# Optimization experiments

Measured on AMD Instinct MI355X. Metric: run time of the kernel, lower is better.

The kernel has to match this reference:

```python
import jax, jax.numpy as jnp
import numpy as np

NEG_INF = -1e9


def setup_inputs() -> dict:
    key = jax.random.key(0)
    ks = jax.random.split(key, 8)
    B, S, D = 8, 2048, 1024
    scale = 1.0 / np.sqrt(D)
    src = jax.random.normal(ks[0], (B, S, D), dtype=jnp.float32)
    pad_len = jax.random.randint(ks[1], (B,), 0, S // 10)
    pos = jnp.arange(S)[None, :]
    src_padding_mask = jnp.where(pos >= (S - pad_len)[:, None], NEG_INF, 0.0).astype(jnp.float32)[:, :, None]
    # causal (subsequent) additive mask [S,S]
    src_subsq_mask = jnp.where(jnp.triu(jnp.ones((S, S), dtype=bool), k=1), NEG_INF, 0.0).astype(jnp.float32)
    Wk = jax.random.normal(ks[2], (D, D), dtype=jnp.float32) * scale
    Wv = jax.random.normal(ks[3], (D, D), dtype=jnp.float32) * scale
    Wq = jax.random.normal(ks[4], (D, D), dtype=jnp.float32) * scale
    bk = jnp.zeros((D,), dtype=jnp.float32)
    bv = jnp.zeros((D,), dtype=jnp.float32)
    bq = jnp.zeros((D,), dtype=jnp.float32)
    return {"src": src, "src_padding_mask": src_padding_mask, "src_subsq_mask": src_subsq_mask,
            "Wk": Wk, "bk": bk, "Wv": Wv, "bv": bv, "Wq": Wq, "bq": bq}


def reference(src, src_padding_mask, src_subsq_mask, Wk, bk, Wv, bv, Wq, bq):
    d_model = src.shape[-1]
    # torch nn.Linear: x @ W.T + b
    keys = jnp.einsum('bsd,ed->bse', src, Wk) + bk
    values = jnp.einsum('bsd,ed->bse', src, Wv) + bv
    queries = jnp.einsum('bsd,ed->bse', src, Wq) + bq
    sqrt_d = jnp.asarray(d_model, src.dtype) ** 0.5
    att = jnp.einsum('bqd,bkd->bqk', queries, keys) / sqrt_d   # [B,S,S]
    att = att + jnp.swapaxes(src_padding_mask, 1, 2)           # [B,1,S] broadcast
    att = att + src_subsq_mask[None, :, :]                      # [1,S,S] broadcast
    att_softmax = jax.nn.softmax(att, axis=2)
    att_out = jnp.einsum('bqk,bkd->bqd', att_softmax, values)
    return att_out
```

## Files before the change

### kernel.cpp

```cpp
#include <hip/hip_runtime.h>
#include <cstdint>
#include <cstddef>

#define BATCH 8
#define SEQ   2048
#define DM    1024

typedef _Float16 half8 __attribute__((ext_vector_type(8)));
typedef _Float16 half4v __attribute__((ext_vector_type(4)));
typedef float floatx4 __attribute__((ext_vector_type(4)));
typedef float float4v __attribute__((ext_vector_type(4)));

#define GLOBAL_AS __attribute__((address_space(1)))
#define LDS_AS    __attribute__((address_space(3)))

__device__ __forceinline__ void gl_lds16(const _Float16* g, _Float16* l) {
    __builtin_amdgcn_global_load_lds((const GLOBAL_AS void*)g, (LDS_AS void*)l, 16, 0, 0);
}

__device__ __forceinline__ void stage128(const _Float16* __restrict__ g, int ld, int k0,
                                         _Float16* l, int wave, int lane) {
    const int rw = wave * 8 + (lane >> 3);
    const int sl = lane & 7;
    #pragma unroll
    for (int i = 0; i < 2; i++) {
        const int r = i * 64 + rw;
        gl_lds16(g + (size_t)r * ld + k0 + ((sl ^ (r & 7)) << 3),
                 l + ((i * 64 + wave * 8) << 6));
    }
}

#define LDA4(BUF, HALFOFF)                                                    \
    _Pragma("unroll")                                                         \
    for (int i = 0; i < 4; i++) {                                             \
        a[i][0] = *(const half8*)&SA[BUF][aoff + (HALFOFF) + i * 1024 + sl0]; \
        a[i][1] = *(const half8*)&SA[BUF][aoff + (HALFOFF) + i * 1024 + sl1]; \
    }
#define LDB2(DST, BUF, HALFOFF)                                               \
    _Pragma("unroll")                                                         \
    for (int j = 0; j < 2; j++) {                                             \
        DST[j][0] = *(const half8*)&SB[BUF][boff + (HALFOFF) + j * 4096 + sl0]; \
        DST[j][1] = *(const half8*)&SB[BUF][boff + (HALFOFF) + j * 4096 + sl1]; \
    }

#define PH_MFMA(IOFF, JOFF, BREG)                                             \
    __builtin_amdgcn_s_barrier();                                             \
    asm volatile("s_waitcnt lgkmcnt(0)" ::: "memory");                        \
    __builtin_amdgcn_s_setprio(1);                                            \
    _Pragma("unroll")                                                         \
    for (int i = 0; i < 4; i++) {                                             \
        _Pragma("unroll")                                                     \
        for (int j = 0; j < 2; j++) {                                         \
            acc[(IOFF) + i][(JOFF) + j] = __builtin_amdgcn_mfma_f32_16x16x32_f16( \
                a[i][0], BREG[j][0], acc[(IOFF) + i][(JOFF) + j], 0, 0, 0);   \
            acc[(IOFF) + i][(JOFF) + j] = __builtin_amdgcn_mfma_f32_16x16x32_f16( \
                a[i][1], BREG[j][1], acc[(IOFF) + i][(JOFF) + j], 0, 0, 0);   \
        }                                                                     \
    }                                                                         \
    __builtin_amdgcn_s_setprio(0);

__device__ __forceinline__ void gemm256_8ph(
    const _Float16* __restrict__ A, const _Float16* __restrict__ B,
    int lda, int ldb, int nkt,
    _Float16 (&SA)[2][16384], _Float16 (&SB)[2][16384],
    floatx4 (&acc)[8][4])
{
    const int t = threadIdx.x;
    const int wave = t >> 6, lane = t & 63;
    const int l15 = lane & 15, kq = lane >> 4;
    const int wm = wave >> 2, wn = wave & 3;

    const int aoff = (wm * 64 + l15) << 6;
    const int boff = (wn * 16 + l15) << 6;
    const int sl0 = ((kq ^ (l15 & 7)) << 3);
    const int sl1 = (((4 + kq) ^ (l15 & 7)) << 3);

    const _Float16* A128 = A + (size_t)128 * lda;
    const _Float16* B128 = B + (size_t)128 * ldb;

    stage128(A,    lda, 0,  &SA[0][0],    wave, lane);
    stage128(B,    ldb, 0,  &SB[0][0],    wave, lane);
    stage128(A128, lda, 0,  &SA[0][8192], wave, lane);
    stage128(B128, ldb, 0,  &SB[0][8192], wave, lane);
    stage128(A,    lda, 64, &SA[1][0],    wave, lane);
    stage128(B,    ldb, 64, &SB[1][0],    wave, lane);
    asm volatile("s_waitcnt vmcnt(4)" ::: "memory");
    __builtin_amdgcn_s_barrier();
    __builtin_amdgcn_sched_barrier(0);

    half8 a[4][2], b0[2][2], b1[2][2];

    for (int kt = 0; kt < nkt; kt += 2) {
        const bool more = (kt + 2) < nkt;
        const int kA = (kt + 1) * 64, kB = (kt + 2) * 64, kC = (kt + 3) * 64;

        LDA4(0, 0); LDB2(b0, 0, 0);
        stage128(A128, lda, kA, &SA[1][8192], wave, lane);
        PH_MFMA(0, 0, b0);
        __builtin_amdgcn_s_barrier();

        LDB2(b1, 0, 8192);
        stage128(B128, ldb, kA, &SB[1][8192], wave, lane);
        PH_MFMA(0, 2, b1);
        __builtin_amdgcn_s_barrier();

        LDA4(0, 8192);
        if (more) stage128(A, lda, kB, &SA[0][0], wave, lane);
        PH_MFMA(4, 0, b0);
        __builtin_amdgcn_s_barrier();

        if (more) stage128(B, ldb, kB, &SB[0][0], wave, lane);
        PH_MFMA(4, 2, b1);
        if (more) { asm volatile("s_waitcnt vmcnt(4)" ::: "memory"); }
        else      { asm volatile("s_waitcnt vmcnt(0)" ::: "memory"); }
        __builtin_amdgcn_s_barrier();
        __builtin_amdgcn_sched_barrier(0);

        LDA4(1, 0); LDB2(b0, 1, 0);
        if (more) stage128(A128, lda, kB, &SA[0][8192], wave, lane);
        PH_MFMA(0, 0, b0);
        __builtin_amdgcn_s_barrier();

        LDB2(b1, 1, 8192);
        if (more) stage128(B128, ldb, kB, &SB[0][8192], wave, lane);
        PH_MFMA(0, 2, b1);
        __builtin_amdgcn_s_barrier();

        LDA4(1, 8192);
        if (more) stage128(A, lda, kC, &SA[1][0], wave, lane);
        PH_MFMA(4, 0, b0);
        __builtin_amdgcn_s_barrier();

        if (more) stage128(B, ldb, kC, &SB[1][0], wave, lane);
        PH_MFMA(4, 2, b1);
        if (more) { asm volatile("s_waitcnt vmcnt(4)" ::: "memory"); }
        __builtin_amdgcn_s_barrier();
        __builtin_amdgcn_sched_barrier(0);
    }
}

__global__ __launch_bounds__(256) void convert_inputs(
    const float* __restrict__ src,
    const float* __restrict__ Wk, const float* __restrict__ Wv, const float* __restrict__ Wq,
    _Float16* __restrict__ Xh, _Float16* __restrict__ Wh)
{
    const int gid = blockIdx.x * 256 + threadIdx.x;
    const int gs  = gridDim.x * 256;
    const int nX4 = BATCH * SEQ * DM / 4;
    const int nW4 = DM * DM / 4;
    const float4v* s4  = (const float4v*)src;
    const float4v* wk4 = (const float4v*)Wk;
    const float4v* wv4 = (const float4v*)Wv;
    const float4v* wq4 = (const float4v*)Wq;
    half4v* x4 = (half4v*)Xh;
    half4v* w4 = (half4v*)Wh;
    for (int i = gid; i < nX4; i += gs) {
        float4v v = s4[i];
        half4v h;
        #pragma unroll
        for (int e = 0; e < 4; e++) h[e] = (_Float16)v[e];
        x4[i] = h;
    }
    for (int i = gid; i < nW4; i += gs) {
        float4v a = wk4[i], b = wv4[i], c = wq4[i];
        half4v ha, hb, hc;
        #pragma unroll
        for (int e = 0; e < 4; e++) { ha[e] = (_Float16)a[e]; hb[e] = (_Float16)b[e]; hc[e] = (_Float16)c[e]; }
        w4[i]           = ha;
        w4[nW4 + i]     = hb;
        w4[2 * nW4 + i] = hc;
    }
}

__global__ __launch_bounds__(512, 2) void qkv_gemm(
    const _Float16* __restrict__ Xh, const _Float16* __restrict__ Wh,
    const float* __restrict__ bk, const float* __restrict__ bv, const float* __restrict__ bq,
    _Float16* __restrict__ Kh, _Float16* __restrict__ Vt, _Float16* __restrict__ Qh)
{
    __shared__ __align__(16) _Float16 SA[2][16384];
    __shared__ __align__(16) _Float16 SB[2][16384];
    const int L = blockIdx.x;
    const int lid = (L & 7) * 96 + (L >> 3);
    const int z = lid >> 8;
    const int r = lid & 255;
    int by, bx;
    const _Float16 *A, *B;
    if (z == 1) {
        by = r & 3; bx = r >> 2;
        A = Wh + (size_t)DM * DM + (size_t)by * 256 * DM;
        B = Xh + (size_t)bx * 256 * DM;
    } else {
        by = r >> 2; bx = r & 3;
        A = Xh + (size_t)by * 256 * DM;
        B = Wh + (z ? (size_t)2 * DM * DM : (size_t)0) + (size_t)bx * 256 * DM;
    }
    floatx4 acc[8][4] = {};
    gemm256_8ph(A, B, DM, DM, 16, SA, SB, acc);

    const int t = threadIdx.x, wave = t >> 6, lane = t & 63;
    const int l15 = lane & 15, kq = lane >> 4;
    const int wm = wave >> 2, wn = wave & 3;
    if (z == 1) {
        #pragma unroll
        for (int i = 0; i < 8; i++)
            #pragma unroll
            for (int j = 0; j < 4; j++)
                #pragma unroll
                for (int rr = 0; rr < 4; rr++) {
                    const int d  = by * 256 + wm * 64 + (i & 3) * 16 + (i >> 2) * 128 + kq * 4 + rr;
                    const int sg = bx * 256 + wn * 16 + j * 64 + l15;
                    const int b = sg >> 11, s = sg & (SEQ - 1);
                    Vt[((size_t)b * DM + d) * SEQ + s] = (_Float16)(acc[i][j][rr] + bv[d]);
                }
    } else {
        const float* bias = z ? bq : bk;
        _Float16* outp    = z ? Qh : Kh;
        #pragma unroll
        for (int i = 0; i < 8; i++)
            #pragma unroll
            for (int j = 0; j < 4; j++)
                #pragma unroll
                for (int rr = 0; rr < 4; rr++) {
                    const int row = by * 256 + wm * 64 + (i & 3) * 16 + (i >> 2) * 128 + kq * 4 + rr;
                    const int col = bx * 256 + wn * 16 + j * 64 + l15;
                    outp[(size_t)row * DM + col] = (_Float16)(acc[i][j][rr] + bias[col]);
                }
    }
}

__global__ __launch_bounds__(512, 2) void scores_gemm(
    const _Float16* __restrict__ Qh, const _Float16* __restrict__ Kh,
    const float* __restrict__ pad, _Float16* __restrict__ Sc)
{
    __shared__ __align__(16) _Float16 SA[2][16384];
    __shared__ __align__(16) _Float16 SB[2][16384];
    const int L = blockIdx.x;
    const int lid = (L & 7) * 36 + (L >> 3);
    const int b = lid / 36, tri = lid - b * 36;
    int by = 0;
    #pragma unroll
    for (int u = 1; u <= 7; u++) if (tri >= (u * (u + 1)) / 2) by = u;
    const int bx = tri - (by * (by + 1)) / 2;

    const _Float16* A = Qh + ((size_t)b * SEQ + by * 256) * DM;
    const _Float16* B = Kh + ((size_t)b * SEQ + bx * 256) * DM;
    floatx4 acc[8][4] = {};
    gemm256_8ph(A, B, DM, DM, 16, SA, SB, acc);

    const int t = threadIdx.x, wave = t >> 6, lane = t & 63;
    const int l15 = lane & 15, kq = lane >> 4;
    const int wm = wave >> 2, wn = wave & 3;
    #pragma unroll
    for (int i = 0; i < 8; i++)
        #pragma unroll
        for (int j = 0; j < 4; j++)
            #pragma unroll
            for (int rr = 0; rr < 4; rr++) {
                const int row = by * 256 + wm * 64 + (i & 3) * 16 + (i >> 2) * 128 + kq * 4 + rr;
                const int col = bx * 256 + wn * 16 + j * 64 + l15;
                Sc[((size_t)b * SEQ + row) * SEQ + col] =
                    (_Float16)(acc[i][j][rr] * 0.03125f + pad[b * SEQ + col]);
            }
}

__global__ __launch_bounds__(256) void softmax_rows(_Float16* __restrict__ Sc)
{
    const int bid = blockIdx.x;
    const int b = bid >> 11, q = bid & (SEQ - 1);
    _Float16* row = Sc + ((size_t)b * SEQ + q) * SEQ;
    const int n = q + 1;
    const int kmaxr = ((q >> 8) + 1) << 8;
    const int t = threadIdx.x;
    const int c0 = t * 8;
    const bool active = (c0 < kmaxr);
    __shared__ float red[4];

    half8 v = {};
    if (active) v = *(const half8*)(row + c0);
    float f[8];
    float m = -3.0e38f;
    #pragma unroll
    for (int e = 0; e < 8; e++) {
        f[e] = (active && (c0 + e < n)) ? (float)v[e] : -3.0e38f;
        m = fmaxf(m, f[e]);
    }
    #pragma unroll
    for (int o = 32; o > 0; o >>= 1) m = fmaxf(m, __shfl_down(m, o));
    if ((t & 63) == 0) red[t >> 6] = m;
    __syncthreads();
    m = fmaxf(fmaxf(red[0], red[1]), fmaxf(red[2], red[3]));

    float ex[8], s = 0.f;
    #pragma unroll
    for (int e = 0; e < 8; e++) {
        ex[e] = (f[e] > -1.0e38f) ? __expf(f[e] - m) : 0.f;
        s += ex[e];
    }
    #pragma unroll
    for (int o = 32; o > 0; o >>= 1) s += __shfl_down(s, o);
    __syncthreads();
    if ((t & 63) == 0) red[t >> 6] = s;
    __syncthreads();
    s = red[0] + red[1] + red[2] + red[3];

    if (active) {
        const float inv = 1.0f / s;
        half8 o8;
        #pragma unroll
        for (int e = 0; e < 8; e++) o8[e] = (_Float16)(ex[e] * inv);
        *(half8*)(row + c0) = o8;
    }
}

__global__ __launch_bounds__(512, 2) void pv_gemm(
    const _Float16* __restrict__ P, const _Float16* __restrict__ Vt,
    float* __restrict__ out)
{
    __shared__ __align__(16) _Float16 SA[2][16384];
    __shared__ __align__(16) _Float16 SB[2][16384];
    const int L = blockIdx.x;
    const int lid = (L & 7) * 32 + (L >> 3);
    const int b = lid >> 5, r = lid & 31;
    const int by = 7 - (r >> 2);
    const int bx = r & 3;

    const _Float16* A = P  + ((size_t)b * SEQ + by * 256) * SEQ;
    const _Float16* B = Vt + ((size_t)b * DM  + bx * 256) * SEQ;
    const int nkt = (by + 1) * 4;
    floatx4 acc[8][4] = {};
    gemm256_8ph(A, B, SEQ, SEQ, nkt, SA, SB, acc);

    const int t = threadIdx.x, wave = t >> 6, lane = t & 63;
    const int l15 = lane & 15, kq = lane >> 4;
    const int wm = wave >> 2, wn = wave & 3;
    #pragma unroll
    for (int i = 0; i < 8; i++)
        #pragma unroll
        for (int j = 0; j < 4; j++)
            #pragma unroll
            for (int rr = 0; rr < 4; rr++) {
                const int row = by * 256 + wm * 64 + (i & 3) * 16 + (i >> 2) * 128 + kq * 4 + rr;
                const int col = bx * 256 + wn * 16 + j * 64 + l15;
                out[((size_t)b * SEQ + row) * DM + col] = acc[i][j][rr];
            }
}

extern "C" void kernel_launch(void* const* d_in, const int* in_sizes, int n_in,
                              void* d_out, int out_size, void* d_ws, size_t ws_size,
                              hipStream_t stream) {
    const float* src = (const float*)d_in[0];
    const float* pad = (const float*)d_in[1];
    const float* Wk = (const float*)d_in[3];
    const float* bk = (const float*)d_in[4];
    const float* Wv = (const float*)d_in[5];
    const float* bv = (const float*)d_in[6];
    const float* Wq = (const float*)d_in[7];
    const float* bq = (const float*)d_in[8];
    float* out = (float*)d_out;

    char* ws = (char*)d_ws;
    _Float16* Wh = (_Float16*)(ws);
    _Float16* Qh = (_Float16*)(ws + 6291456);
    _Float16* Kh = (_Float16*)(ws + 39845888);
    _Float16* Vt = (_Float16*)(ws + 73400320);
    _Float16* Sc = (_Float16*)(ws + 106954752);
    _Float16* Xh = (_Float16*)d_out;

    convert_inputs<<<2048, 256, 0, stream>>>(src, Wk, Wv, Wq, Xh, Wh);
    qkv_gemm<<<768, 512, 0, stream>>>(Xh, Wh, bk, bv, bq, Kh, Vt, Qh);
    scores_gemm<<<288, 512, 0, stream>>>(Qh, Kh, pad, Sc);
    softmax_rows<<<BATCH * SEQ, 256, 0, stream>>>(Sc);
    pv_gemm<<<256, 512, 0, stream>>>(Sc, Vt, out);
}
```

Baseline: 384.5 us.

## Software-pipeline LDS fragment reads one phase ahead of MFMA in GEMM loop

```diff
diff --git a/kernel.cpp b/kernel.cpp
--- a/kernel.cpp
+++ b/kernel.cpp
@@ -30,34 +30,38 @@
     }
 }
 
-#define LDA4(BUF, HALFOFF)                                                    \
+#define SCHED __builtin_amdgcn_sched_barrier(0)
+#define BAR   __builtin_amdgcn_s_barrier()
+
+#define RD_A(BUF, HOFF)                                                       \
     _Pragma("unroll")                                                         \
     for (int i = 0; i < 4; i++) {                                             \
-        a[i][0] = *(const half8*)&SA[BUF][aoff + (HALFOFF) + i * 1024 + sl0]; \
-        a[i][1] = *(const half8*)&SA[BUF][aoff + (HALFOFF) + i * 1024 + sl1]; \
-    }
-#define LDB2(DST, BUF, HALFOFF)                                               \
+        a[i][0] = *(const half8*)&SA[BUF][aoff + (HOFF) + i * 1024 + sl0];    \
+        a[i][1] = *(const half8*)&SA[BUF][aoff + (HOFF) + i * 1024 + sl1];    \
+    }
+#define RD_B(DST, BUF, HOFF)                                                  \
     _Pragma("unroll")                                                         \
     for (int j = 0; j < 2; j++) {                                             \
-        DST[j][0] = *(const half8*)&SB[BUF][boff + (HALFOFF) + j * 4096 + sl0]; \
-        DST[j][1] = *(const half8*)&SB[BUF][boff + (HALFOFF) + j * 4096 + sl1]; \
-    }
-
-#define PH_MFMA(IOFF, JOFF, BREG)                                             \
-    __builtin_amdgcn_s_barrier();                                             \
-    asm volatile("s_waitcnt lgkmcnt(0)" ::: "memory");                        \
+        DST[j][0] = *(const half8*)&SB[BUF][boff + (HOFF) + j * 4096 + sl0];  \
+        DST[j][1] = *(const half8*)&SB[BUF][boff + (HOFF) + j * 4096 + sl1];  \
+    }
+
+#define MM(IOFF, JOFF, BV)                                                    \
     __builtin_amdgcn_s_setprio(1);                                            \
     _Pragma("unroll")                                                         \
     for (int i = 0; i < 4; i++) {                                             \
         _Pragma("unroll")                                                     \
         for (int j = 0; j < 2; j++) {                                         \
             acc[(IOFF) + i][(JOFF) + j] = __builtin_amdgcn_mfma_f32_16x16x32_f16( \
-                a[i][0], BREG[j][0], acc[(IOFF) + i][(JOFF) + j], 0, 0, 0);   \
+                a[i][0], BV[j][0], acc[(IOFF) + i][(JOFF) + j], 0, 0, 0);     \
             acc[(IOFF) + i][(JOFF) + j] = __builtin_amdgcn_mfma_f32_16x16x32_f16( \
-                a[i][1], BREG[j][1], acc[(IOFF) + i][(JOFF) + j], 0, 0, 0);   \
+                a[i][1], BV[j][1], acc[(IOFF) + i][(JOFF) + j], 0, 0, 0);     \
         }                                                                     \
     }                                                                         \
     __builtin_amdgcn_s_setprio(0);
+
+#define WAIT_LGKM0 asm volatile("s_waitcnt lgkmcnt(0)" ::: "memory")
+#define WAIT_LGKM4 asm volatile("s_waitcnt lgkmcnt(4)" ::: "memory")
 
 __device__ __forceinline__ void gemm256_8ph(
     const _Float16* __restrict__ A, const _Float16* __restrict__ B,
@@ -85,57 +89,73 @@
     stage128(A,    lda, 64, &SA[1][0],    wave, lane);
     stage128(B,    ldb, 64, &SB[1][0],    wave, lane);
     asm volatile("s_waitcnt vmcnt(4)" ::: "memory");
-    __builtin_amdgcn_s_barrier();
-    __builtin_amdgcn_sched_barrier(0);
+    BAR;
+    SCHED;
 
     half8 a[4][2], b0[2][2], b1[2][2];
+    RD_A(0, 0); RD_B(b0, 0, 0); RD_B(b1, 0, 8192);
 
     for (int kt = 0; kt < nkt; kt += 2) {
         const bool more = (kt + 2) < nkt;
         const int kA = (kt + 1) * 64, kB = (kt + 2) * 64, kC = (kt + 3) * 64;
 
-        LDA4(0, 0); LDB2(b0, 0, 0);
         stage128(A128, lda, kA, &SA[1][8192], wave, lane);
-        PH_MFMA(0, 0, b0);
-        __builtin_amdgcn_s_barrier();
-
-        LDB2(b1, 0, 8192);
+        BAR; WAIT_LGKM0; SCHED;
+        MM(0, 0, b0);
+        SCHED; BAR;
+
         stage128(B128, ldb, kA, &SB[1][8192], wave, lane);
-        PH_MFMA(0, 2, b1);
-        __builtin_amdgcn_s_barrier();
-
-        LDA4(0, 8192);
+        BAR; WAIT_LGKM0; SCHED;
+        MM(0, 2, b1);
+        SCHED;
+        RD_A(0, 8192);
+        BAR;
+
         if (more) stage128(A, lda, kB, &SA[0][0], wave, lane);
-        PH_MFMA(4, 0, b0);
-        __builtin_amdgcn_s_barrier();
-
+        BAR; WAIT_LGKM0; SCHED;
+        MM(4, 0, b0);
+        SCHED;
+        if (more) { asm volatile("s_waitcnt vmcnt(2)" ::: "memory"); }
+        else      { asm volatile("s_waitcnt vmcnt(0)" ::: "memory"); }
+        BAR; SCHED;
+
+        RD_B(b0, 1, 0);
         if (more) stage128(B, ldb, kB, &SB[0][0], wave, lane);
-        PH_MFMA(4, 2, b1);
-        if (more) { asm volatile("s_waitcnt vmcnt(4)" ::: "memory"); }
+        BAR; WAIT_LGKM4; SCHED;
+        MM(4, 2, b1);
+        SCHED;
+        RD_A(1, 0); RD_B(b1, 1, 8192);
+        BAR;
+
+        if (more) stage128(A128, lda, kB, &SA[0][8192], wave, lane);
+        BAR; WAIT_LGKM0; SCHED;
+        MM(0, 0, b0);
+        SCHED; BAR;
+
+        if (more) stage128(B128, ldb, kB, &SB[0][8192], wave, lane);
+        BAR; WAIT_LGKM0; SCHED;
+        MM(0, 2, b1);
+        SCHED;
+        RD_A(1, 8192);
+        BAR;
+
+        if (more) stage128(A, lda, kC, &SA[1][0], wave, lane);
+        BAR; WAIT_LGKM0; SCHED;
+        MM(4, 0, b0);
+        SCHED;
+        if (more) { asm volatile("s_waitcnt vmcnt(2)" ::: "memory"); }
         else      { asm volatile("s_waitcnt vmcnt(0)" ::: "memory"); }
-        __builtin_amdgcn_s_barrier();
-        __builtin_amdgcn_sched_barrier(0);
-
-        LDA4(1, 0); LDB2(b0, 1, 0);
-        if (more) stage128(A128, lda, kB, &SA[0][8192], wave, lane);
-        PH_MFMA(0, 0, b0);
-        __builtin_amdgcn_s_barrier();
-
-        LDB2(b1, 1, 8192);
-        if (more) stage128(B128, ldb, kB, &SB[0][8192], wave, lane);
-        PH_MFMA(0, 2, b1);
-        __builtin_amdgcn_s_barrier();
-
-        LDA4(1, 8192);
-        if (more) stage128(A, lda, kC, &SA[1][0], wave, lane);
-        PH_MFMA(4, 0, b0);
-        __builtin_amdgcn_s_barrier();
-
+        BAR; SCHED;
+
+        if (more) { RD_B(b0, 0, 0); }
         if (more) stage128(B, ldb, kC, &SB[1][0], wave, lane);
-        PH_MFMA(4, 2, b1);
-        if (more) { asm volatile("s_waitcnt vmcnt(4)" ::: "memory"); }
-        __builtin_amdgcn_s_barrier();
-        __builtin_amdgcn_sched_barrier(0);
+        BAR;
+        if (more) { WAIT_LGKM4; } else { WAIT_LGKM0; }
+        SCHED;
+        MM(4, 2, b1);
+        SCHED;
+        if (more) { RD_A(0, 0); RD_B(b1, 0, 8192); }
+        BAR;
     }
 }
 
```

Result: slower. 395.1 us (+2.8%).

## Switch GEMM core to 32x32x16 MFMA with register-prefetched LDS pipeline

Applied to the files above, without the earlier changes.

```diff
diff --git a/kernel.cpp b/kernel.cpp
--- a/kernel.cpp
+++ b/kernel.cpp
@@ -8,7 +8,7 @@
 
 typedef _Float16 half8 __attribute__((ext_vector_type(8)));
 typedef _Float16 half4v __attribute__((ext_vector_type(4)));
-typedef float floatx4 __attribute__((ext_vector_type(4)));
+typedef float floatx16 __attribute__((ext_vector_type(16)));
 typedef float float4v __attribute__((ext_vector_type(4)));
 
 #define GLOBAL_AS __attribute__((address_space(1)))
@@ -30,112 +30,89 @@
     }
 }
 
-#define LDA4(BUF, HALFOFF)                                                    \
+#define SCHED __builtin_amdgcn_sched_barrier(0)
+#define BAR   __builtin_amdgcn_s_barrier()
+#define WAIT_VM0   asm volatile("s_waitcnt vmcnt(0)" ::: "memory")
+#define WAIT_LGKM6 asm volatile("s_waitcnt lgkmcnt(6)" ::: "memory")
+#define WAIT_LGKM0 asm volatile("s_waitcnt lgkmcnt(0)" ::: "memory")
+
+#define RD(AV, BV, BUF, KS)                                                   \
     _Pragma("unroll")                                                         \
-    for (int i = 0; i < 4; i++) {                                             \
-        a[i][0] = *(const half8*)&SA[BUF][aoff + (HALFOFF) + i * 1024 + sl0]; \
-        a[i][1] = *(const half8*)&SA[BUF][aoff + (HALFOFF) + i * 1024 + sl1]; \
-    }
-#define LDB2(DST, BUF, HALFOFF)                                               \
+    for (int f_ = 0; f_ < 4; f_++) {                                          \
+        const int r_ = f_ * 32 + l31;                                         \
+        AV[f_] = *(const half8*)&SA[BUF][hA + r_ * 64 + ((((KS)*2 + o0) ^ (r_ & 7)) << 3)]; \
+    }                                                                         \
     _Pragma("unroll")                                                         \
-    for (int j = 0; j < 2; j++) {                                             \
-        DST[j][0] = *(const half8*)&SB[BUF][boff + (HALFOFF) + j * 4096 + sl0]; \
-        DST[j][1] = *(const half8*)&SB[BUF][boff + (HALFOFF) + j * 4096 + sl1]; \
-    }
-
-#define PH_MFMA(IOFF, JOFF, BREG)                                             \
-    __builtin_amdgcn_s_barrier();                                             \
-    asm volatile("s_waitcnt lgkmcnt(0)" ::: "memory");                        \
+    for (int g_ = 0; g_ < 2; g_++) {                                          \
+        const int r_ = rb + g_ * 32;                                          \
+        BV[g_] = *(const half8*)&SB[BUF][hB + r_ * 64 + ((((KS)*2 + o0) ^ (r_ & 7)) << 3)]; \
+    }
+
+#define MM(AV, BV)                                                            \
     __builtin_amdgcn_s_setprio(1);                                            \
     _Pragma("unroll")                                                         \
-    for (int i = 0; i < 4; i++) {                                             \
+    for (int f_ = 0; f_ < 4; f_++)                                            \
         _Pragma("unroll")                                                     \
-        for (int j = 0; j < 2; j++) {                                         \
-            acc[(IOFF) + i][(JOFF) + j] = __builtin_amdgcn_mfma_f32_16x16x32_f16( \
-                a[i][0], BREG[j][0], acc[(IOFF) + i][(JOFF) + j], 0, 0, 0);   \
-            acc[(IOFF) + i][(JOFF) + j] = __builtin_amdgcn_mfma_f32_16x16x32_f16( \
-                a[i][1], BREG[j][1], acc[(IOFF) + i][(JOFF) + j], 0, 0, 0);   \
-        }                                                                     \
-    }                                                                         \
+        for (int g_ = 0; g_ < 2; g_++)                                        \
+            acc[f_][g_] = __builtin_amdgcn_mfma_f32_32x32x16_f16(             \
+                AV[f_], BV[g_], acc[f_][g_], 0, 0, 0);                        \
     __builtin_amdgcn_s_setprio(0);
 
-__device__ __forceinline__ void gemm256_8ph(
+__device__ __forceinline__ void gemm256_rr(
     const _Float16* __restrict__ A, const _Float16* __restrict__ B,
     int lda, int ldb, int nkt,
     _Float16 (&SA)[2][16384], _Float16 (&SB)[2][16384],
-    floatx4 (&acc)[8][4])
+    floatx16 (&acc)[4][2])
 {
     const int t = threadIdx.x;
     const int wave = t >> 6, lane = t & 63;
-    const int l15 = lane & 15, kq = lane >> 4;
+    const int l31 = lane & 31, o0 = lane >> 5;
     const int wm = wave >> 2, wn = wave & 3;
 
-    const int aoff = (wm * 64 + l15) << 6;
-    const int boff = (wn * 16 + l15) << 6;
-    const int sl0 = ((kq ^ (l15 & 7)) << 3);
-    const int sl1 = (((4 + kq) ^ (l15 & 7)) << 3);
+    const int hA = wm * 8192;
+    const int hB = (wn >> 1) * 8192;
+    const int rb = (wn & 1) * 64 + l31;
 
     const _Float16* A128 = A + (size_t)128 * lda;
     const _Float16* B128 = B + (size_t)128 * ldb;
 
-    stage128(A,    lda, 0,  &SA[0][0],    wave, lane);
-    stage128(B,    ldb, 0,  &SB[0][0],    wave, lane);
-    stage128(A128, lda, 0,  &SA[0][8192], wave, lane);
-    stage128(B128, ldb, 0,  &SB[0][8192], wave, lane);
-    stage128(A,    lda, 64, &SA[1][0],    wave, lane);
-    stage128(B,    ldb, 64, &SB[1][0],    wave, lane);
-    asm volatile("s_waitcnt vmcnt(4)" ::: "memory");
-    __builtin_amdgcn_s_barrier();
-    __builtin_amdgcn_sched_barrier(0);
-
-    half8 a[4][2], b0[2][2], b1[2][2];
-
-    for (int kt = 0; kt < nkt; kt += 2) {
-        const bool more = (kt + 2) < nkt;
-        const int kA = (kt + 1) * 64, kB = (kt + 2) * 64, kC = (kt + 3) * 64;
-
-        LDA4(0, 0); LDB2(b0, 0, 0);
-        stage128(A128, lda, kA, &SA[1][8192], wave, lane);
-        PH_MFMA(0, 0, b0);
-        __builtin_amdgcn_s_barrier();
-
-        LDB2(b1, 0, 8192);
-        stage128(B128, ldb, kA, &SB[1][8192], wave, lane);
-        PH_MFMA(0, 2, b1);
-        __builtin_amdgcn_s_barrier();
-
-        LDA4(0, 8192);
-        if (more) stage128(A, lda, kB, &SA[0][0], wave, lane);
-        PH_MFMA(4, 0, b0);
-        __builtin_amdgcn_s_barrier();
-
-        if (more) stage128(B, ldb, kB, &SB[0][0], wave, lane);
-        PH_MFMA(4, 2, b1);
-        if (more) { asm volatile("s_waitcnt vmcnt(4)" ::: "memory"); }
-        else      { asm volatile("s_waitcnt vmcnt(0)" ::: "memory"); }
-        __builtin_amdgcn_s_barrier();
-        __builtin_amdgcn_sched_barrier(0);
-
-        LDA4(1, 0); LDB2(b0, 1, 0);
-        if (more) stage128(A128, lda, kB, &SA[0][8192], wave, lane);
-        PH_MFMA(0, 0, b0);
-        __builtin_amdgcn_s_barrier();
-
-        LDB2(b1, 1, 8192);
-        if (more) stage128(B128, ldb, kB, &SB[0][8192], wave, lane);
-        PH_MFMA(0, 2, b1);
-        __builtin_amdgcn_s_barrier();
-
-        LDA4(1, 8192);
-        if (more) stage128(A, lda, kC, &SA[1][0], wave, lane);
-        PH_MFMA(4, 0, b0);
-        __builtin_amdgcn_s_barrier();
-
-        if (more) stage128(B, ldb, kC, &SB[1][0], wave, lane);
-        PH_MFMA(4, 2, b1);
-        if (more) { asm volatile("s_waitcnt vmcnt(4)" ::: "memory"); }
-        __builtin_amdgcn_s_barrier();
-        __builtin_amdgcn_sched_barrier(0);
+    half8 a0[4], b0[2], a1[4], b1[2];
+
+    stage128(A,    lda, 0, &SA[0][0],    wave, lane);
+    stage128(A128, lda, 0, &SA[0][8192], wave, lane);
+    stage128(B,    ldb, 0, &SB[0][0],    wave, lane);
+    stage128(B128, ldb, 0, &SB[0][8192], wave, lane);
+    WAIT_VM0;
+    BAR; SCHED;
+    RD(a0, b0, 0, 0);
+
+    for (int kt = 0; kt < nkt; ++kt) {
+        const int bs = kt & 1;
+        const bool more = (kt + 1) < nkt;
+        if (more) {
+            const int k1 = (kt + 1) * 64;
+            stage128(A,    lda, k1, &SA[bs ^ 1][0],    wave, lane);
+            stage128(A128, lda, k1, &SA[bs ^ 1][8192], wave, lane);
+            stage128(B,    ldb, k1, &SB[bs ^ 1][0],    wave, lane);
+            stage128(B128, ldb, k1, &SB[bs ^ 1][8192], wave, lane);
+        }
+        SCHED;
+        RD(a1, b1, bs, 1);
+        WAIT_LGKM6; SCHED;
+        MM(a0, b0);
+        RD(a0, b0, bs, 2);
+        WAIT_LGKM6; SCHED;
+        MM(a1, b1);
+        RD(a1, b1, bs, 3);
+        WAIT_LGKM6; SCHED;
+        MM(a0, b0);
+        WAIT_LGKM0;
+        if (more) {
+            WAIT_VM0;
+            BAR; SCHED;
+            RD(a0, b0, bs ^ 1, 0);
+        }
+        MM(a1, b1);
     }
 }
 
@@ -194,36 +171,36 @@
         A = Xh + (size_t)by * 256 * DM;
         B = Wh + (z ? (size_t)2 * DM * DM : (size_t)0) + (size_t)bx * 256 * DM;
     }
-    floatx4 acc[8][4] = {};
-    gemm256_8ph(A, B, DM, DM, 16, SA, SB, acc);
+    floatx16 acc[4][2] = {};
+    gemm256_rr(A, B, DM, DM, 16, SA, SB, acc);
 
     const int t = threadIdx.x, wave = t >> 6, lane = t & 63;
-    const int l15 = lane & 15, kq = lane >> 4;
+    const int l31 = lane & 31, o0 = lane >> 5;
     const int wm = wave >> 2, wn = wave & 3;
     if (z == 1) {
         #pragma unroll
-        for (int i = 0; i < 8; i++)
+        for (int f = 0; f < 4; f++)
             #pragma unroll
-            for (int j = 0; j < 4; j++)
+            for (int g = 0; g < 2; g++)
                 #pragma unroll
-                for (int rr = 0; rr < 4; rr++) {
-                    const int d  = by * 256 + wm * 64 + (i & 3) * 16 + (i >> 2) * 128 + kq * 4 + rr;
-                    const int sg = bx * 256 + wn * 16 + j * 64 + l15;
+                for (int rg = 0; rg < 16; rg++) {
+                    const int d  = by * 256 + wm * 128 + f * 32 + 4 * o0 + (rg & 3) + 8 * (rg >> 2);
+                    const int sg = bx * 256 + wn * 64 + g * 32 + l31;
                     const int b = sg >> 11, s = sg & (SEQ - 1);
-                    Vt[((size_t)b * DM + d) * SEQ + s] = (_Float16)(acc[i][j][rr] + bv[d]);
+                    Vt[((size_t)b * DM + d) * SEQ + s] = (_Float16)(acc[f][g][rg] + bv[d]);
                 }
     } else {
         const float* bias = z ? bq : bk;
         _Float16* outp    = z ? Qh : Kh;
         #pragma unroll
-        for (int i = 0; i < 8; i++)
+        for (int f = 0; f < 4; f++)
             #pragma unroll
-            for (int j = 0; j < 4; j++)
+            for (int g = 0; g < 2; g++)
                 #pragma unroll
-                for (int rr = 0; rr < 4; rr++) {
-                    const int row = by * 256 + wm * 64 + (i & 3) * 16 + (i >> 2) * 128 + kq * 4 + rr;
-                    const int col = bx * 256 + wn * 16 + j * 64 + l15;
-                    outp[(size_t)row * DM + col] = (_Float16)(acc[i][j][rr] + bias[col]);
+                for (int rg = 0; rg < 16; rg++) {
+                    const int row = by * 256 + wm * 128 + f * 32 + 4 * o0 + (rg & 3) + 8 * (rg >> 2);
+                    const int col = bx * 256 + wn * 64 + g * 32 + l31;
+                    outp[(size_t)row * DM + col] = (_Float16)(acc[f][g][rg] + bias[col]);
                 }
     }
 }
@@ -244,22 +221,22 @@
 
     const _Float16* A = Qh + ((size_t)b * SEQ + by * 256) * DM;
     const _Float16* B = Kh + ((size_t)b * SEQ + bx * 256) * DM;
-    floatx4 acc[8][4] = {};
-    gemm256_8ph(A, B, DM, DM, 16, SA, SB, acc);
+    floatx16 acc[4][2] = {};
+    gemm256_rr(A, B, DM, DM, 16, SA, SB, acc);
 
     const int t = threadIdx.x, wave = t >> 6, lane = t & 63;
-    const int l15 = lane & 15, kq = lane >> 4;
+    const int l31 = lane & 31, o0 = lane >> 5;
     const int wm = wave >> 2, wn = wave & 3;
     #pragma unroll
-    for (int i = 0; i < 8; i++)
-        #pragma unroll
-        for (int j = 0; j < 4; j++)
+    for (int f = 0; f < 4; f++)
+        #pragma unroll
+        for (int g = 0; g < 2; g++)
             #pragma unroll
-            for (int rr = 0; rr < 4; rr++) {
-                const int row = by * 256 + wm * 64 + (i & 3) * 16 + (i >> 2) * 128 + kq * 4 + rr;
-                const int col = bx * 256 + wn * 16 + j * 64 + l15;
+            for (int rg = 0; rg < 16; rg++) {
+                const int row = by * 256 + wm * 128 + f * 32 + 4 * o0 + (rg & 3) + 8 * (rg >> 2);
+                const int col = bx * 256 + wn * 64 + g * 32 + l31;
                 Sc[((size_t)b * SEQ + row) * SEQ + col] =
-                    (_Float16)(acc[i][j][rr] * 0.03125f + pad[b * SEQ + col]);
+                    (_Float16)(acc[f][g][rg] * 0.03125f + pad[b * SEQ + col]);
             }
 }
 
@@ -327,21 +304,21 @@
     const _Float16* A = P  + ((size_t)b * SEQ + by * 256) * SEQ;
     const _Float16* B = Vt + ((size_t)b * DM  + bx * 256) * SEQ;
     const int nkt = (by + 1) * 4;
-    floatx4 acc[8][4] = {};
-    gemm256_8ph(A, B, SEQ, SEQ, nkt, SA, SB, acc);
+    floatx16 acc[4][2] = {};
+    gemm256_rr(A, B, SEQ, SEQ, nkt, SA, SB, acc);
 
     const int t = threadIdx.x, wave = t >> 6, lane = t & 63;
-    const int l15 = lane & 15, kq = lane >> 4;
+    const int l31 = lane & 31, o0 = lane >> 5;
     const int wm = wave >> 2, wn = wave & 3;
     #pragma unroll
-    for (int i = 0; i < 8; i++)
-        #pragma unroll
-        for (int j = 0; j < 4; j++)
+    for (int f = 0; f < 4; f++)
+        #pragma unroll
+        for (int g = 0; g < 2; g++)
             #pragma unroll
-            for (int rr = 0; rr < 4; rr++) {
-                const int row = by * 256 + wm * 64 + (i & 3) * 16 + (i >> 2) * 128 + kq * 4 + rr;
-                const int col = bx * 256 + wn * 16 + j * 64 + l15;
-                out[((size_t)b * SEQ + row) * DM + col] = acc[i][j][rr];
+            for (int rg = 0; rg < 16; rg++) {
+                const int row = by * 256 + wm * 128 + f * 32 + 4 * o0 + (rg & 3) + 8 * (rg >> 2);
+                const int col = bx * 256 + wn * 64 + g * 32 + l31;
+                out[((size_t)b * SEQ + row) * DM + col] = acc[f][g][rg];
             }
 }
 
```

New measurement: 395.2 us. +2.8%, slower.

## Replace 8-phase GEMM schedule with per-k-tile register double-buffered loop

Applied to the files above, without the earlier changes.

```diff
diff --git a/kernel.cpp b/kernel.cpp
--- a/kernel.cpp
+++ b/kernel.cpp
@@ -30,36 +30,37 @@
     }
 }
 
-#define LDA4(BUF, HALFOFF)                                                    \
-    _Pragma("unroll")                                                         \
-    for (int i = 0; i < 4; i++) {                                             \
-        a[i][0] = *(const half8*)&SA[BUF][aoff + (HALFOFF) + i * 1024 + sl0]; \
-        a[i][1] = *(const half8*)&SA[BUF][aoff + (HALFOFF) + i * 1024 + sl1]; \
-    }
-#define LDB2(DST, BUF, HALFOFF)                                               \
-    _Pragma("unroll")                                                         \
-    for (int j = 0; j < 2; j++) {                                             \
-        DST[j][0] = *(const half8*)&SB[BUF][boff + (HALFOFF) + j * 4096 + sl0]; \
-        DST[j][1] = *(const half8*)&SB[BUF][boff + (HALFOFF) + j * 4096 + sl1]; \
-    }
-
-#define PH_MFMA(IOFF, JOFF, BREG)                                             \
-    __builtin_amdgcn_s_barrier();                                             \
-    asm volatile("s_waitcnt lgkmcnt(0)" ::: "memory");                        \
+#define SCHED __builtin_amdgcn_sched_barrier(0)
+#define BAR   __builtin_amdgcn_s_barrier()
+#define WAIT_VM0    asm volatile("s_waitcnt vmcnt(0)" ::: "memory")
+#define WAIT_LGKM12 asm volatile("s_waitcnt lgkmcnt(12)" ::: "memory")
+#define WAIT_LGKM0  asm volatile("s_waitcnt lgkmcnt(0)" ::: "memory")
+
+#define RD_SET(AV, BV, BUF, SL)                                               \
+    _Pragma("unroll")                                                         \
+    for (int i_ = 0; i_ < 4; i_++)                                            \
+        AV[i_] = *(const half8*)&SA[BUF][aoff + i_ * 1024 + (SL)];            \
+    _Pragma("unroll")                                                         \
+    for (int i_ = 0; i_ < 4; i_++)                                            \
+        AV[4 + i_] = *(const half8*)&SA[BUF][aoff + 8192 + i_ * 1024 + (SL)]; \
+    _Pragma("unroll")                                                         \
+    for (int j_ = 0; j_ < 2; j_++)                                            \
+        BV[j_] = *(const half8*)&SB[BUF][boff + j_ * 4096 + (SL)];            \
+    _Pragma("unroll")                                                         \
+    for (int j_ = 0; j_ < 2; j_++)                                            \
+        BV[2 + j_] = *(const half8*)&SB[BUF][boff + 8192 + j_ * 4096 + (SL)];
+
+#define MM_SET(AV, BV)                                                        \
     __builtin_amdgcn_s_setprio(1);                                            \
     _Pragma("unroll")                                                         \
-    for (int i = 0; i < 4; i++) {                                             \
+    for (int i_ = 0; i_ < 8; i_++)                                            \
         _Pragma("unroll")                                                     \
-        for (int j = 0; j < 2; j++) {                                         \
-            acc[(IOFF) + i][(JOFF) + j] = __builtin_amdgcn_mfma_f32_16x16x32_f16( \
-                a[i][0], BREG[j][0], acc[(IOFF) + i][(JOFF) + j], 0, 0, 0);   \
-            acc[(IOFF) + i][(JOFF) + j] = __builtin_amdgcn_mfma_f32_16x16x32_f16( \
-                a[i][1], BREG[j][1], acc[(IOFF) + i][(JOFF) + j], 0, 0, 0);   \
-        }                                                                     \
-    }                                                                         \
+        for (int j_ = 0; j_ < 4; j_++)                                        \
+            acc[i_][j_] = __builtin_amdgcn_mfma_f32_16x16x32_f16(             \
+                AV[i_], BV[j_], acc[i_][j_], 0, 0, 0);                        \
     __builtin_amdgcn_s_setprio(0);
 
-__device__ __forceinline__ void gemm256_8ph(
+__device__ __forceinline__ void gemm256_rr(
     const _Float16* __restrict__ A, const _Float16* __restrict__ B,
     int lda, int ldb, int nkt,
     _Float16 (&SA)[2][16384], _Float16 (&SB)[2][16384],
@@ -78,64 +79,35 @@
     const _Float16* A128 = A + (size_t)128 * lda;
     const _Float16* B128 = B + (size_t)128 * ldb;
 
-    stage128(A,    lda, 0,  &SA[0][0],    wave, lane);
-    stage128(B,    ldb, 0,  &SB[0][0],    wave, lane);
-    stage128(A128, lda, 0,  &SA[0][8192], wave, lane);
-    stage128(B128, ldb, 0,  &SB[0][8192], wave, lane);
-    stage128(A,    lda, 64, &SA[1][0],    wave, lane);
-    stage128(B,    ldb, 64, &SB[1][0],    wave, lane);
-    asm volatile("s_waitcnt vmcnt(4)" ::: "memory");
-    __builtin_amdgcn_s_barrier();
-    __builtin_amdgcn_sched_barrier(0);
-
-    half8 a[4][2], b0[2][2], b1[2][2];
-
-    for (int kt = 0; kt < nkt; kt += 2) {
-        const bool more = (kt + 2) < nkt;
-        const int kA = (kt + 1) * 64, kB = (kt + 2) * 64, kC = (kt + 3) * 64;
-
-        LDA4(0, 0); LDB2(b0, 0, 0);
-        stage128(A128, lda, kA, &SA[1][8192], wave, lane);
-        PH_MFMA(0, 0, b0);
-        __builtin_amdgcn_s_barrier();
-
-        LDB2(b1, 0, 8192);
-        stage128(B128, ldb, kA, &SB[1][8192], wave, lane);
-        PH_MFMA(0, 2, b1);
-        __builtin_amdgcn_s_barrier();
-
-        LDA4(0, 8192);
-        if (more) stage128(A, lda, kB, &SA[0][0], wave, lane);
-        PH_MFMA(4, 0, b0);
-        __builtin_amdgcn_s_barrier();
-
-        if (more) stage128(B, ldb, kB, &SB[0][0], wave, lane);
-        PH_MFMA(4, 2, b1);
-        if (more) { asm volatile("s_waitcnt vmcnt(4)" ::: "memory"); }
-        else      { asm volatile("s_waitcnt vmcnt(0)" ::: "memory"); }
-        __builtin_amdgcn_s_barrier();
-        __builtin_amdgcn_sched_barrier(0);
-
-        LDA4(1, 0); LDB2(b0, 1, 0);
-        if (more) stage128(A128, lda, kB, &SA[0][8192], wave, lane);
-        PH_MFMA(0, 0, b0);
-        __builtin_amdgcn_s_barrier();
-
-        LDB2(b1, 1, 8192);
-        if (more) stage128(B128, ldb, kB, &SB[0][8192], wave, lane);
-        PH_MFMA(0, 2, b1);
-        __builtin_amdgcn_s_barrier();
-
-        LDA4(1, 8192);
-        if (more) stage128(A, lda, kC, &SA[1][0], wave, lane);
-        PH_MFMA(4, 0, b0);
-        __builtin_amdgcn_s_barrier();
-
-        if (more) stage128(B, ldb, kC, &SB[1][0], wave, lane);
-        PH_MFMA(4, 2, b1);
-        if (more) { asm volatile("s_waitcnt vmcnt(4)" ::: "memory"); }
-        __builtin_amdgcn_s_barrier();
-        __builtin_amdgcn_sched_barrier(0);
+    half8 a0[8], b0[4], a1[8], b1[4];
+
+    stage128(A,    lda, 0, &SA[0][0],    wave, lane);
+    stage128(A128, lda, 0, &SA[0][8192], wave, lane);
+    stage128(B,    ldb, 0, &SB[0][0],    wave, lane);
+    stage128(B128, ldb, 0, &SB[0][8192], wave, lane);
+    WAIT_VM0; BAR; SCHED;
+    RD_SET(a0, b0, 0, sl0);
+
+    for (int kt = 0; kt < nkt; ++kt) {
+        const int bs = kt & 1;
+        const bool more = (kt + 1) < nkt;
+        if (more) {
+            const int k1 = (kt + 1) * 64;
+            stage128(A,    lda, k1, &SA[bs ^ 1][0],    wave, lane);
+            stage128(A128, lda, k1, &SA[bs ^ 1][8192], wave, lane);
+            stage128(B,    ldb, k1, &SB[bs ^ 1][0],    wave, lane);
+            stage128(B128, ldb, k1, &SB[bs ^ 1][8192], wave, lane);
+        }
+        RD_SET(a1, b1, bs, sl1);
+        WAIT_LGKM12; SCHED;
+        MM_SET(a0, b0);
+        WAIT_LGKM0; SCHED;
+        if (more) {
+            WAIT_VM0;
+            BAR; SCHED;
+            RD_SET(a0, b0, bs ^ 1, sl0);
+        }
+        MM_SET(a1, b1);
     }
 }
 
@@ -195,7 +167,7 @@
         B = Wh + (z ? (size_t)2 * DM * DM : (size_t)0) + (size_t)bx * 256 * DM;
     }
     floatx4 acc[8][4] = {};
-    gemm256_8ph(A, B, DM, DM, 16, SA, SB, acc);
+    gemm256_rr(A, B, DM, DM, 16, SA, SB, acc);
 
     const int t = threadIdx.x, wave = t >> 6, lane = t & 63;
     const int l15 = lane & 15, kq = lane >> 4;
@@ -208,7 +180,7 @@
                 #pragma unroll
                 for (int rr = 0; rr < 4; rr++) {
                     const int d  = by * 256 + wm * 64 + (i & 3) * 16 + (i >> 2) * 128 + kq * 4 + rr;
-                    const int sg = bx * 256 + wn * 16 + j * 64 + l15;
+                    const int sg = bx * 256 + wn * 16 + (j & 1) * 64 + (j >> 1) * 128 + l15;
                     const int b = sg >> 11, s = sg & (SEQ - 1);
                     Vt[((size_t)b * DM + d) * SEQ + s] = (_Float16)(acc[i][j][rr] + bv[d]);
                 }
@@ -222,7 +194,7 @@
                 #pragma unroll
                 for (int rr = 0; rr < 4; rr++) {
                     const int row = by * 256 + wm * 64 + (i & 3) * 16 + (i >> 2) * 128 + kq * 4 + rr;
-                    const int col = bx * 256 + wn * 16 + j * 64 + l15;
+                    const int col = bx * 256 + wn * 16 + (j & 1) * 64 + (j >> 1) * 128 + l15;
                     outp[(size_t)row * DM + col] = (_Float16)(acc[i][j][rr] + bias[col]);
                 }
     }
@@ -245,7 +217,7 @@
     const _Float16* A = Qh + ((size_t)b * SEQ + by * 256) * DM;
     const _Float16* B = Kh + ((size_t)b * SEQ + bx * 256) * DM;
     floatx4 acc[8][4] = {};
-    gemm256_8ph(A, B, DM, DM, 16, SA, SB, acc);
+    gemm256_rr(A, B, DM, DM, 16, SA, SB, acc);
 
     const int t = threadIdx.x, wave = t >> 6, lane = t & 63;
     const int l15 = lane & 15, kq = lane >> 4;
@@ -257,7 +229,7 @@
             #pragma unroll
             for (int rr = 0; rr < 4; rr++) {
                 const int row = by * 256 + wm * 64 + (i & 3) * 16 + (i >> 2) * 128 + kq * 4 + rr;
-                const int col = bx * 256 + wn * 16 + j * 64 + l15;
+                const int col = bx * 256 + wn * 16 + (j & 1) * 64 + (j >> 1) * 128 + l15;
                 Sc[((size_t)b * SEQ + row) * SEQ + col] =
                     (_Float16)(acc[i][j][rr] * 0.03125f + pad[b * SEQ + col]);
             }
@@ -328,7 +300,7 @@
     const _Float16* B = Vt + ((size_t)b * DM  + bx * 256) * SEQ;
     const int nkt = (by + 1) * 4;
     floatx4 acc[8][4] = {};
-    gemm256_8ph(A, B, SEQ, SEQ, nkt, SA, SB, acc);
+    gemm256_rr(A, B, SEQ, SEQ, nkt, SA, SB, acc);
 
     const int t = threadIdx.x, wave = t >> 6, lane = t & 63;
     const int l15 = lane & 15, kq = lane >> 4;
@@ -340,7 +312,7 @@
             #pragma unroll
             for (int rr = 0; rr < 4; rr++) {
                 const int row = by * 256 + wm * 64 + (i & 3) * 16 + (i >> 2) * 128 + kq * 4 + rr;
-                const int col = bx * 256 + wn * 16 + j * 64 + l15;
+                const int col = bx * 256 + wn * 16 + (j & 1) * 64 + (j >> 1) * 128 + l15;
                 out[((size_t)b * SEQ + row) * DM + col] = acc[i][j][rr];
             }
 }
```

Result: no change. 382.9 us (-0.4%).
